# Performance work log

Measured on AMD Instinct MI355X. Metric: run time of the kernel, lower is better.

Reference implementation:

```python
import jax, jax.numpy as jnp
import numpy as np

C = 64
CR = C // 16  # reduction=16 -> query/key channels
B, H, W = 2, 80, 80


def setup_inputs() -> dict:
    key = jax.random.key(0)
    ks = jax.random.split(key, 13)
    s = 0.05
    return {
        "a": jax.random.normal(ks[0], (B, C, H, W), jnp.float32),
        "b": jax.random.normal(ks[1], (B, C, H, W), jnp.float32),
        "c": jax.random.normal(ks[2], (B, C, H, W), jnp.float32),
        # attentionAB (queries from a, keys from b)
        "wq_ab": jax.random.normal(ks[3], (CR, C), jnp.float32) * s,
        "bq_ab": jax.random.normal(ks[4], (CR,), jnp.float32) * s,
        "wk_ab": jax.random.normal(ks[5], (CR, C), jnp.float32) * s,
        "bk_ab": jax.random.normal(ks[6], (CR,), jnp.float32) * s,
        # attentionBC (queries from c, keys from b)
        "wq_bc": jax.random.normal(ks[7], (CR, C), jnp.float32) * s,
        "bq_bc": jax.random.normal(ks[8], (CR,), jnp.float32) * s,
        "wk_bc": jax.random.normal(ks[9], (CR, C), jnp.float32) * s,
        "bk_bc": jax.random.normal(ks[10], (CR,), jnp.float32) * s,
        # outer value conv on b
        "wv": jax.random.normal(ks[11], (C, C), jnp.float32) * s,
        "bv": jax.random.normal(ks[12], (C,), jnp.float32) * s,
    }


def _proj(x_flat, w, bias):
    # conv1x1 on flattened [B, C, N] -> [B, D, N]
    return jnp.einsum("dc,bcn->bdn", w, x_flat) + bias[None, :, None]


def _attention(x1_flat, x2_flat, wq, bq, wk, bk):
    q = _proj(x1_flat, wq, bq)  # [B, CR, N1]
    k = _proj(x2_flat, wk, bk)  # [B, CR, N2]
    scores = jnp.einsum("bdn,bdm->bnm", q, k)  # [B, N1, N2]
    return jax.nn.softmax(scores, axis=-1)


def reference(a, b, c, wq_ab, bq_ab, wk_ab, bk_ab, wq_bc, bq_bc, wk_bc, bk_bc, wv, bv):
    bsz, ch, h, w = b.shape
    n = h * w
    af = a.reshape(bsz, ch, n)
    bf = b.reshape(bsz, ch, n)
    cf = c.reshape(bsz, ch, n)

    attn_ba = _attention(af, bf, wq_ab, bq_ab, wk_ab, bk_ab)  # [B, Na, Nb]
    attn_bc = _attention(cf, bf, wq_bc, bq_bc, wk_bc, bk_bc)  # [B, Nc, Nb]

    values_b = _proj(bf, wv, bv)  # [B, C, Nb]

    # bmm(values_b, attn^T): contract over key positions m (of b)
    enh_ba = jnp.einsum("bcm,bnm->bcn", values_b, attn_ba)
    enh_bc = jnp.einsum("bcm,bnm->bcn", values_b, attn_bc)
    enhanced = (enh_ba + enh_bc) * 0.5
    return enhanced.reshape(bsz, ch, h, w)
```

## Files before the change

### kernel.cpp

```cpp
#include <hip/hip_runtime.h>
#include <hip/hip_bf16.h>

#define NPIX 6400
#define LOG2E 1.44269504088896340736f
#define KH 5
#define KEYS 1280
#define NCH 20
#define QF 2
#define VSTRIDE 136

typedef _Float16 half_t;
typedef _Float16 half4 __attribute__((ext_vector_type(4)));
typedef __fp16 fp16x2 __attribute__((ext_vector_type(2)));
typedef float float4x __attribute__((ext_vector_type(4)));
typedef unsigned long long u64;

__device__ __forceinline__ float fast_exp2(float x) {
    float r;
    asm volatile("v_exp_f32 %0, %1" : "=v"(r) : "v"(x));
    return r;
}

__global__ __launch_bounds__(256) void proj_kernel(
    const float* __restrict__ a, const float* __restrict__ b, const float* __restrict__ c,
    const float* __restrict__ wq_ab, const float* __restrict__ bq_ab,
    const float* __restrict__ wk_ab, const float* __restrict__ bk_ab,
    const float* __restrict__ wq_bc, const float* __restrict__ bq_bc,
    const float* __restrict__ wk_bc, const float* __restrict__ bk_bc,
    const float* __restrict__ wv, const float* __restrict__ bvb,
    half_t* __restrict__ qp, half_t* __restrict__ kp, half_t* __restrict__ vp,
    float* __restrict__ num)
{
    int bid = blockIdx.x;
    if (bid < 400) {
        int tid = bid * 256 + threadIdx.x;
        int n4 = tid % 1600;
        int cc = (tid / 1600) & 31;
        int bz = tid / (1600 * 32);
        const float* B = b + bz * 64 * NPIX + n4 * 4;
        float b0 = bvb[cc], b1 = bvb[cc + 32];
        float4x acc0 = {b0, b0, b0, b0}, acc1 = {b1, b1, b1, b1};
        for (int ch = 0; ch < 64; ++ch) {
            float4x bv = *(const float4x*)(B + ch * NPIX);
            acc0 += wv[cc * 64 + ch] * bv;
            acc1 += wv[(cc + 32) * 64 + ch] * bv;
        }
        half4 h0 = {(half_t)acc0[0], (half_t)acc0[1], (half_t)acc0[2], (half_t)acc0[3]};
        half4 h1 = {(half_t)acc1[0], (half_t)acc1[1], (half_t)acc1[2], (half_t)acc1[3]};
        *(half4*)(vp + (bz * 64 + cc) * NPIX + n4 * 4) = h0;
        *(half4*)(vp + (bz * 64 + cc + 32) * NPIX + n4 * 4) = h1;
    } else if (bid < 600) {
        int tid = (bid - 400) * 256 + threadIdx.x;
        int d = tid & 3;
        int n = (tid >> 2) % NPIX;
        int bz = (tid >> 2) / NPIX;
        const float* A = a + bz * 64 * NPIX + n;
        const float* B = b + bz * 64 * NPIX + n;
        const float* C = c + bz * 64 * NPIX + n;
        float qab = 0.f, kab = 0.f, qbc = 0.f, kbc = 0.f;
#pragma unroll 4
        for (int ch = 0; ch < 64; ++ch) {
            float av = A[ch * NPIX], bv = B[ch * NPIX], cv = C[ch * NPIX];
            qab += wq_ab[d * 64 + ch] * av;
            kab += wk_ab[d * 64 + ch] * bv;
            qbc += wq_bc[d * 64 + ch] * cv;
            kbc += wk_bc[d * 64 + ch] * bv;
        }
        qp[((bz * 2 + 0) * NPIX + n) * 4 + d] = (half_t)((qab + bq_ab[d]) * LOG2E);
        qp[((bz * 2 + 1) * NPIX + n) * 4 + d] = (half_t)((qbc + bq_bc[d]) * LOG2E);
        kp[((bz * 2 + 0) * NPIX + n) * 4 + d] = (half_t)(kab + bk_ab[d]);
        kp[((bz * 2 + 1) * NPIX + n) * 4 + d] = (half_t)(kbc + bk_bc[d]);
    } else {
        int tid = (bid - 600) * 256 + threadIdx.x;
        float4x z = {0.f, 0.f, 0.f, 0.f};
        float4x* p = (float4x*)num;
        for (int i = tid; i < 416000; i += 25600) p[i] = z;
    }
}

__global__ __launch_bounds__(256) void attn_kernel(
    const half_t* __restrict__ qp, const half_t* __restrict__ kp,
    const half_t* __restrict__ vp, float* __restrict__ num, float* __restrict__ lsum)
{
    int bid = blockIdx.x;
    int swz = (bid & 7) * 125 + (bid >> 3);
    int qc = swz % 50;
    int br = (swz / 50) & 1;
    int bz = (swz / 100) & 1;
    int kh = swz / 200;

    int tid = threadIdx.x;
    int lane = tid & 63, w = tid >> 6;
    int g = lane >> 4, qi = lane & 15;
    int qbase = qc * 128 + w * 32;

    const half_t* Q = qp + ((bz * 2 + br) * NPIX + qbase) * 4;
    const half_t* K = kp + ((bz * 2 + br) * NPIX + kh * KEYS) * 4;
    const half_t* V = vp + bz * 64 * NPIX + kh * KEYS;

    half4 hz = {(half_t)0, (half_t)0, (half_t)0, (half_t)0};
    half4 qf[QF];
#pragma unroll
    for (int i = 0; i < QF; ++i)
        qf[i] = (lane < 16) ? *(const half4*)(Q + (i * 16 + lane) * 4) : hz;

    float4x accs[QF][4] = {{{0,0,0,0},{0,0,0,0},{0,0,0,0},{0,0,0,0}},
                           {{0,0,0,0},{0,0,0,0},{0,0,0,0},{0,0,0,0}}};
    float lrun[QF] = {0.f, 0.f};

    __shared__ char lds[2][64 * VSTRIDE];

    u64 vpre[4];
#pragma unroll
    for (int p = 0; p < 4; ++p) {
        int idx = p * 256 + tid; int row = idx >> 4, w4 = idx & 15;
        vpre[p] = *(const u64*)(V + row * NPIX + w4 * 4);
    }
    half4 kc[4];
#pragma unroll
    for (int t = 0; t < 4; ++t)
        kc[t] = (lane < 16) ? *(const half4*)(K + (t * 16 + lane) * 4) : hz;
#pragma unroll
    for (int p = 0; p < 4; ++p) {
        int idx = p * 256 + tid; int row = idx >> 4, w4 = idx & 15;
        *(u64*)(lds[0] + row * VSTRIDE + w4 * 8) = vpre[p];
    }
    __syncthreads();

    int cur = 0;
    for (int chn = 0; chn < NCH; ++chn) {
        bool more = (chn + 1 < NCH);
        u64 vn[4];
        half4 kn[4];
        if (more) {
            int m0n = (chn + 1) * 64;
#pragma unroll
            for (int p = 0; p < 4; ++p) {
                int idx = p * 256 + tid; int row = idx >> 4, w4 = idx & 15;
                vn[p] = *(const u64*)(V + row * NPIX + m0n + w4 * 4);
            }
#pragma unroll
            for (int t = 0; t < 4; ++t)
                kn[t] = (lane < 16) ? *(const half4*)(K + (m0n + t * 16 + lane) * 4) : hz;
        }
        const char* lb = lds[cur];
        half4 vfa[4], vfb[4];
#pragma unroll
        for (int cb = 0; cb < 4; ++cb)
            vfa[cb] = *(const half4*)(lb + (cb * 16 + qi) * VSTRIDE + g * 8);
#pragma unroll
        for (int t = 0; t < 4; ++t) {
            half4* vcur = (t & 1) ? vfb : vfa;
            half4* vnxt = (t & 1) ? vfa : vfb;
            if (t < 3) {
#pragma unroll
                for (int cb = 0; cb < 4; ++cb)
                    vnxt[cb] = *(const half4*)(lb + (cb * 16 + qi) * VSTRIDE + (t + 1) * 32 + g * 8);
            }
#pragma unroll
            for (int i = 0; i < QF; ++i) {
                float4x zero = {0.f, 0.f, 0.f, 0.f};
                float4x sc = __builtin_amdgcn_mfma_f32_16x16x16f16(kc[t], qf[i], zero, 0, 0, 0);
                float p0 = fast_exp2(sc[0]), p1 = fast_exp2(sc[1]);
                float p2 = fast_exp2(sc[2]), p3 = fast_exp2(sc[3]);
                lrun[i] += (p0 + p1) + (p2 + p3);
                union { fp16x2 h2[2]; half4 h4; } pk;
                pk.h2[0] = __builtin_amdgcn_cvt_pkrtz(p0, p1);
                pk.h2[1] = __builtin_amdgcn_cvt_pkrtz(p2, p3);
                half4 pf = pk.h4;
#pragma unroll
                for (int cb = 0; cb < 4; ++cb)
                    accs[i][cb] = __builtin_amdgcn_mfma_f32_16x16x16f16(vcur[cb], pf, accs[i][cb], 0, 0, 0);
            }
        }
        if (more) {
#pragma unroll
            for (int p = 0; p < 4; ++p) {
                int idx = p * 256 + tid; int row = idx >> 4, w4 = idx & 15;
                *(u64*)(lds[cur ^ 1] + row * VSTRIDE + w4 * 8) = vn[p];
            }
#pragma unroll
            for (int t = 0; t < 4; ++t) kc[t] = kn[t];
        }
        __syncthreads();
        cur ^= 1;
    }

    float* numb = num + (bz * 2 + br) * 64 * NPIX;
#pragma unroll
    for (int i = 0; i < QF; ++i) {
        float l = lrun[i];
        l += __shfl_xor(l, 16, 64);
        l += __shfl_xor(l, 32, 64);
        int q = qbase + i * 16 + qi;
        if (g == 0) atomicAdd(&lsum[(bz * 2 + br) * NPIX + q], l);
#pragma unroll
        for (int cb = 0; cb < 4; ++cb)
#pragma unroll
            for (int r = 0; r < 4; ++r)
                atomicAdd(&numb[(cb * 16 + 4 * g + r) * NPIX + q], accs[i][cb][r]);
    }
}

__global__ __launch_bounds__(256) void norm_kernel(
    const float* __restrict__ num, const float* __restrict__ lsum, float* __restrict__ out)
{
    int tid = blockIdx.x * 256 + threadIdx.x;
    int n4 = tid % 1600;
    int c  = (tid / 1600) & 63;
    int bz = tid / (1600 * 64);
    float4x lA = *(const float4x*)(lsum + (bz * 2 + 0) * NPIX + n4 * 4);
    float4x lC = *(const float4x*)(lsum + (bz * 2 + 1) * NPIX + n4 * 4);
    float4x vA = *(const float4x*)(num + ((bz * 2 + 0) * 64 + c) * NPIX + n4 * 4);
    float4x vC = *(const float4x*)(num + ((bz * 2 + 1) * 64 + c) * NPIX + n4 * 4);
    float4x r;
#pragma unroll
    for (int j = 0; j < 4; ++j)
        r[j] = 0.5f * (vA[j] * __builtin_amdgcn_rcpf(lA[j]) +
                       vC[j] * __builtin_amdgcn_rcpf(lC[j]));
    *(float4x*)(out + (bz * 64 + c) * NPIX + n4 * 4) = r;
}

extern "C" void kernel_launch(void* const* d_in, const int* in_sizes, int n_in,
                              void* d_out, int out_size, void* d_ws, size_t ws_size,
                              hipStream_t stream) {
    (void)in_sizes; (void)n_in; (void)out_size; (void)ws_size;
    const float* a     = (const float*)d_in[0];
    const float* b     = (const float*)d_in[1];
    const float* c     = (const float*)d_in[2];
    const float* wq_ab = (const float*)d_in[3];
    const float* bq_ab = (const float*)d_in[4];
    const float* wk_ab = (const float*)d_in[5];
    const float* bk_ab = (const float*)d_in[6];
    const float* wq_bc = (const float*)d_in[7];
    const float* bq_bc = (const float*)d_in[8];
    const float* wk_bc = (const float*)d_in[9];
    const float* bk_bc = (const float*)d_in[10];
    const float* wv    = (const float*)d_in[11];
    const float* bv    = (const float*)d_in[12];
    float* out = (float*)d_out;

    half_t* qp = (half_t*)d_ws;
    half_t* kp = qp + 2 * 2 * NPIX * 4;
    half_t* vp = kp + 2 * 2 * NPIX * 4;
    float* num  = (float*)(vp + 2 * 64 * NPIX);
    float* lsum = num + 2 * 2 * 64 * NPIX;

    proj_kernel<<<700, 256, 0, stream>>>(a, b, c, wq_ab, bq_ab, wk_ab, bk_ab,
                                         wq_bc, bq_bc, wk_bc, bk_bc, wv, bv,
                                         qp, kp, vp, num);
    attn_kernel<<<1000, 256, 0, stream>>>(qp, kp, vp, num, lsum);
    norm_kernel<<<800, 256, 0, stream>>>(num, lsum, out);
}
```

Before: 193.7 us.

## Use MFMA for projections and drop LDS staging in attention kernel

The projection kernel now computes the Q/K/V 1x1 convolutions with fp16 MFMA instructions, one wave per 16 pixels, instead of scalar FMA loops. The attention kernel loads V and K fragments straight from global memory into registers with a one-step prefetch, removing the LDS double buffer and the __syncthreads. Keys are split into 10 chunks instead of 5, doubling the grid to raise parallelism at the cost of more atomic adds into num. Rounding inputs and weights to fp16 in the projections lowers precision.

Result: slower. 259.1 us (+33.7%).

```diff
diff --git a/kernel.cpp b/kernel.cpp
--- a/kernel.cpp
+++ b/kernel.cpp
@@ -3,22 +3,27 @@
 
 #define NPIX 6400
 #define LOG2E 1.44269504088896340736f
-#define KH 5
-#define KEYS 1280
-#define NCH 20
+#define KH 10
+#define KEYS 640
+#define NSTEP 40
 #define QF 2
-#define VSTRIDE 136
 
 typedef _Float16 half_t;
 typedef _Float16 half4 __attribute__((ext_vector_type(4)));
 typedef __fp16 fp16x2 __attribute__((ext_vector_type(2)));
 typedef float float4x __attribute__((ext_vector_type(4)));
-typedef unsigned long long u64;
 
 __device__ __forceinline__ float fast_exp2(float x) {
     float r;
     asm volatile("v_exp_f32 %0, %1" : "=v"(r) : "v"(x));
     return r;
+}
+
+__device__ __forceinline__ half4 cvtf4(float4x v) {
+    union { fp16x2 h2[2]; half4 h4; } u;
+    u.h2[0] = __builtin_amdgcn_cvt_pkrtz(v[0], v[1]);
+    u.h2[1] = __builtin_amdgcn_cvt_pkrtz(v[2], v[3]);
+    return u.h4;
 }
 
 __global__ __launch_bounds__(256) void proj_kernel(
@@ -32,49 +37,88 @@
     float* __restrict__ num)
 {
     int bid = blockIdx.x;
-    if (bid < 400) {
-        int tid = bid * 256 + threadIdx.x;
-        int n4 = tid % 1600;
-        int cc = (tid / 1600) & 31;
-        int bz = tid / (1600 * 32);
-        const float* B = b + bz * 64 * NPIX + n4 * 4;
-        float b0 = bvb[cc], b1 = bvb[cc + 32];
-        float4x acc0 = {b0, b0, b0, b0}, acc1 = {b1, b1, b1, b1};
-        for (int ch = 0; ch < 64; ++ch) {
-            float4x bv = *(const float4x*)(B + ch * NPIX);
-            acc0 += wv[cc * 64 + ch] * bv;
-            acc1 += wv[(cc + 32) * 64 + ch] * bv;
-        }
-        half4 h0 = {(half_t)acc0[0], (half_t)acc0[1], (half_t)acc0[2], (half_t)acc0[3]};
-        half4 h1 = {(half_t)acc1[0], (half_t)acc1[1], (half_t)acc1[2], (half_t)acc1[3]};
-        *(half4*)(vp + (bz * 64 + cc) * NPIX + n4 * 4) = h0;
-        *(half4*)(vp + (bz * 64 + cc + 32) * NPIX + n4 * 4) = h1;
-    } else if (bid < 600) {
-        int tid = (bid - 400) * 256 + threadIdx.x;
-        int d = tid & 3;
-        int n = (tid >> 2) % NPIX;
-        int bz = (tid >> 2) / NPIX;
-        const float* A = a + bz * 64 * NPIX + n;
-        const float* B = b + bz * 64 * NPIX + n;
-        const float* C = c + bz * 64 * NPIX + n;
-        float qab = 0.f, kab = 0.f, qbc = 0.f, kbc = 0.f;
-#pragma unroll 4
-        for (int ch = 0; ch < 64; ++ch) {
-            float av = A[ch * NPIX], bv = B[ch * NPIX], cv = C[ch * NPIX];
-            qab += wq_ab[d * 64 + ch] * av;
-            kab += wk_ab[d * 64 + ch] * bv;
-            qbc += wq_bc[d * 64 + ch] * cv;
-            kbc += wk_bc[d * 64 + ch] * bv;
-        }
-        qp[((bz * 2 + 0) * NPIX + n) * 4 + d] = (half_t)((qab + bq_ab[d]) * LOG2E);
-        qp[((bz * 2 + 1) * NPIX + n) * 4 + d] = (half_t)((qbc + bq_bc[d]) * LOG2E);
-        kp[((bz * 2 + 0) * NPIX + n) * 4 + d] = (half_t)(kab + bk_ab[d]);
-        kp[((bz * 2 + 1) * NPIX + n) * 4 + d] = (half_t)(kbc + bk_bc[d]);
-    } else {
-        int tid = (bid - 600) * 256 + threadIdx.x;
+    int tid = threadIdx.x;
+    if (bid >= 200) {
+        int t = (bid - 200) * 256 + tid;
         float4x z = {0.f, 0.f, 0.f, 0.f};
         float4x* p = (float4x*)num;
-        for (int i = tid; i < 416000; i += 25600) p[i] = z;
+        for (int i = t; i < 416000; i += 16384) p[i] = z;
+        return;
+    }
+    int wid = bid * 4 + (tid >> 6);
+    int lane = tid & 63;
+    int m = lane & 15, g = lane >> 4;
+    int bz = wid / 400;
+    int pix0 = (wid % 400) * 16;
+    const float* Ain = a + bz * 64 * NPIX + pix0 + m;
+    const float* Bin = b + bz * 64 * NPIX + pix0 + m;
+    const float* Cin = c + bz * 64 * NPIX + pix0 + m;
+
+    float4x zf = {0.f, 0.f, 0.f, 0.f};
+    float4x acc_qa = zf, acc_k = zf, acc_qc = zf;
+    float4x acc_v0 = zf, acc_v1 = zf, acc_v2 = zf, acc_v3 = zf;
+    half4 hz = {(half_t)0, (half_t)0, (half_t)0, (half_t)0};
+
+#pragma unroll
+    for (int kt = 0; kt < 4; ++kt) {
+        int ch0 = kt * 16 + g * 4;
+        float4x fa, fb, fc;
+#pragma unroll
+        for (int j = 0; j < 4; ++j) {
+            fa[j] = Ain[(ch0 + j) * NPIX];
+            fb[j] = Bin[(ch0 + j) * NPIX];
+            fc[j] = Cin[(ch0 + j) * NPIX];
+        }
+        half4 ba = cvtf4(fa), bb = cvtf4(fb), bc_ = cvtf4(fc);
+        half4 wa = hz, w0 = hz, wc = hz;
+        if (m < 4) {
+            wa = cvtf4(*(const float4x*)(wq_ab + m * 64 + ch0));
+            w0 = cvtf4(*(const float4x*)(wk_ab + m * 64 + ch0));
+            wc = cvtf4(*(const float4x*)(wq_bc + m * 64 + ch0));
+        } else if (m < 8) {
+            w0 = cvtf4(*(const float4x*)(wk_bc + (m - 4) * 64 + ch0));
+        }
+        acc_qa = __builtin_amdgcn_mfma_f32_16x16x16f16(wa, ba, acc_qa, 0, 0, 0);
+        acc_k  = __builtin_amdgcn_mfma_f32_16x16x16f16(w0, bb, acc_k, 0, 0, 0);
+        acc_qc = __builtin_amdgcn_mfma_f32_16x16x16f16(wc, bc_, acc_qc, 0, 0, 0);
+        half4 wv0 = cvtf4(*(const float4x*)(wv + (0 * 16 + m) * 64 + ch0));
+        acc_v0 = __builtin_amdgcn_mfma_f32_16x16x16f16(wv0, bb, acc_v0, 0, 0, 0);
+        half4 wv1 = cvtf4(*(const float4x*)(wv + (1 * 16 + m) * 64 + ch0));
+        acc_v1 = __builtin_amdgcn_mfma_f32_16x16x16f16(wv1, bb, acc_v1, 0, 0, 0);
+        half4 wv2 = cvtf4(*(const float4x*)(wv + (2 * 16 + m) * 64 + ch0));
+        acc_v2 = __builtin_amdgcn_mfma_f32_16x16x16f16(wv2, bb, acc_v2, 0, 0, 0);
+        half4 wv3 = cvtf4(*(const float4x*)(wv + (3 * 16 + m) * 64 + ch0));
+        acc_v3 = __builtin_amdgcn_mfma_f32_16x16x16f16(wv3, bb, acc_v3, 0, 0, 0);
+    }
+
+    int px = pix0 + m;
+    if (g == 0) {
+        half4 q0, q1, k0;
+#pragma unroll
+        for (int r = 0; r < 4; ++r) {
+            q0[r] = (half_t)((acc_qa[r] + bq_ab[r]) * LOG2E);
+            q1[r] = (half_t)((acc_qc[r] + bq_bc[r]) * LOG2E);
+            k0[r] = (half_t)(acc_k[r] + bk_ab[r]);
+        }
+        *(half4*)(qp + ((bz * 2 + 0) * NPIX + px) * 4) = q0;
+        *(half4*)(qp + ((bz * 2 + 1) * NPIX + px) * 4) = q1;
+        *(half4*)(kp + ((bz * 2 + 0) * NPIX + px) * 4) = k0;
+    } else if (g == 1) {
+        half4 k1;
+#pragma unroll
+        for (int r = 0; r < 4; ++r) k1[r] = (half_t)(acc_k[r] + bk_bc[r]);
+        *(half4*)(kp + ((bz * 2 + 1) * NPIX + px) * 4) = k1;
+    }
+#pragma unroll
+    for (int r = 0; r < 4; ++r) {
+        int c0 = 0 * 16 + 4 * g + r;
+        vp[(bz * 64 + c0) * NPIX + px] = (half_t)(acc_v0[r] + bvb[c0]);
+        int c1 = 1 * 16 + 4 * g + r;
+        vp[(bz * 64 + c1) * NPIX + px] = (half_t)(acc_v1[r] + bvb[c1]);
+        int c2 = 2 * 16 + 4 * g + r;
+        vp[(bz * 64 + c2) * NPIX + px] = (half_t)(acc_v2[r] + bvb[c2]);
+        int c3 = 3 * 16 + 4 * g + r;
+        vp[(bz * 64 + c3) * NPIX + px] = (half_t)(acc_v3[r] + bvb[c3]);
     }
 }
 
@@ -83,7 +127,7 @@
     const half_t* __restrict__ vp, float* __restrict__ num, float* __restrict__ lsum)
 {
     int bid = blockIdx.x;
-    int swz = (bid & 7) * 125 + (bid >> 3);
+    int swz = (bid & 7) * 250 + (bid >> 3);
     int qc = swz % 50;
     int br = (swz / 50) & 1;
     int bz = (swz / 100) & 1;
@@ -108,82 +152,40 @@
                            {{0,0,0,0},{0,0,0,0},{0,0,0,0},{0,0,0,0}}};
     float lrun[QF] = {0.f, 0.f};
 
-    __shared__ char lds[2][64 * VSTRIDE];
-
-    u64 vpre[4];
-#pragma unroll
-    for (int p = 0; p < 4; ++p) {
-        int idx = p * 256 + tid; int row = idx >> 4, w4 = idx & 15;
-        vpre[p] = *(const u64*)(V + row * NPIX + w4 * 4);
-    }
-    half4 kc[4];
-#pragma unroll
-    for (int t = 0; t < 4; ++t)
-        kc[t] = (lane < 16) ? *(const half4*)(K + (t * 16 + lane) * 4) : hz;
-#pragma unroll
-    for (int p = 0; p < 4; ++p) {
-        int idx = p * 256 + tid; int row = idx >> 4, w4 = idx & 15;
-        *(u64*)(lds[0] + row * VSTRIDE + w4 * 8) = vpre[p];
-    }
-    __syncthreads();
-
-    int cur = 0;
-    for (int chn = 0; chn < NCH; ++chn) {
-        bool more = (chn + 1 < NCH);
-        u64 vn[4];
-        half4 kn[4];
+    half4 kc = (lane < 16) ? *(const half4*)(K + lane * 4) : hz;
+    half4 vc0 = *(const half4*)(V + (0 * 16 + qi) * NPIX + g * 4);
+    half4 vc1 = *(const half4*)(V + (1 * 16 + qi) * NPIX + g * 4);
+    half4 vc2 = *(const half4*)(V + (2 * 16 + qi) * NPIX + g * 4);
+    half4 vc3 = *(const half4*)(V + (3 * 16 + qi) * NPIX + g * 4);
+
+    for (int ts = 0; ts < NSTEP; ++ts) {
+        bool more = (ts + 1 < NSTEP);
+        half4 kn = hz, vn0, vn1, vn2, vn3;
         if (more) {
-            int m0n = (chn + 1) * 64;
-#pragma unroll
-            for (int p = 0; p < 4; ++p) {
-                int idx = p * 256 + tid; int row = idx >> 4, w4 = idx & 15;
-                vn[p] = *(const u64*)(V + row * NPIX + m0n + w4 * 4);
-            }
-#pragma unroll
-            for (int t = 0; t < 4; ++t)
-                kn[t] = (lane < 16) ? *(const half4*)(K + (m0n + t * 16 + lane) * 4) : hz;
-        }
-        const char* lb = lds[cur];
-        half4 vfa[4], vfb[4];
-#pragma unroll
-        for (int cb = 0; cb < 4; ++cb)
-            vfa[cb] = *(const half4*)(lb + (cb * 16 + qi) * VSTRIDE + g * 8);
-#pragma unroll
-        for (int t = 0; t < 4; ++t) {
-            half4* vcur = (t & 1) ? vfb : vfa;
-            half4* vnxt = (t & 1) ? vfa : vfb;
-            if (t < 3) {
-#pragma unroll
-                for (int cb = 0; cb < 4; ++cb)
-                    vnxt[cb] = *(const half4*)(lb + (cb * 16 + qi) * VSTRIDE + (t + 1) * 32 + g * 8);
-            }
-#pragma unroll
-            for (int i = 0; i < QF; ++i) {
-                float4x zero = {0.f, 0.f, 0.f, 0.f};
-                float4x sc = __builtin_amdgcn_mfma_f32_16x16x16f16(kc[t], qf[i], zero, 0, 0, 0);
-                float p0 = fast_exp2(sc[0]), p1 = fast_exp2(sc[1]);
-                float p2 = fast_exp2(sc[2]), p3 = fast_exp2(sc[3]);
-                lrun[i] += (p0 + p1) + (p2 + p3);
-                union { fp16x2 h2[2]; half4 h4; } pk;
-                pk.h2[0] = __builtin_amdgcn_cvt_pkrtz(p0, p1);
-                pk.h2[1] = __builtin_amdgcn_cvt_pkrtz(p2, p3);
-                half4 pf = pk.h4;
-#pragma unroll
-                for (int cb = 0; cb < 4; ++cb)
-                    accs[i][cb] = __builtin_amdgcn_mfma_f32_16x16x16f16(vcur[cb], pf, accs[i][cb], 0, 0, 0);
-            }
-        }
-        if (more) {
-#pragma unroll
-            for (int p = 0; p < 4; ++p) {
-                int idx = p * 256 + tid; int row = idx >> 4, w4 = idx & 15;
-                *(u64*)(lds[cur ^ 1] + row * VSTRIDE + w4 * 8) = vn[p];
-            }
-#pragma unroll
-            for (int t = 0; t < 4; ++t) kc[t] = kn[t];
-        }
-        __syncthreads();
-        cur ^= 1;
+            int mt = (ts + 1) * 16;
+            kn = (lane < 16) ? *(const half4*)(K + (mt + lane) * 4) : hz;
+            vn0 = *(const half4*)(V + (0 * 16 + qi) * NPIX + mt + g * 4);
+            vn1 = *(const half4*)(V + (1 * 16 + qi) * NPIX + mt + g * 4);
+            vn2 = *(const half4*)(V + (2 * 16 + qi) * NPIX + mt + g * 4);
+            vn3 = *(const half4*)(V + (3 * 16 + qi) * NPIX + mt + g * 4);
+        }
+#pragma unroll
+        for (int i = 0; i < QF; ++i) {
+            float4x zero = {0.f, 0.f, 0.f, 0.f};
+            float4x sc = __builtin_amdgcn_mfma_f32_16x16x16f16(kc, qf[i], zero, 0, 0, 0);
+            float p0 = fast_exp2(sc[0]), p1 = fast_exp2(sc[1]);
+            float p2 = fast_exp2(sc[2]), p3 = fast_exp2(sc[3]);
+            lrun[i] += (p0 + p1) + (p2 + p3);
+            union { fp16x2 h2[2]; half4 h4; } pk;
+            pk.h2[0] = __builtin_amdgcn_cvt_pkrtz(p0, p1);
+            pk.h2[1] = __builtin_amdgcn_cvt_pkrtz(p2, p3);
+            half4 pf = pk.h4;
+            accs[i][0] = __builtin_amdgcn_mfma_f32_16x16x16f16(vc0, pf, accs[i][0], 0, 0, 0);
+            accs[i][1] = __builtin_amdgcn_mfma_f32_16x16x16f16(vc1, pf, accs[i][1], 0, 0, 0);
+            accs[i][2] = __builtin_amdgcn_mfma_f32_16x16x16f16(vc2, pf, accs[i][2], 0, 0, 0);
+            accs[i][3] = __builtin_amdgcn_mfma_f32_16x16x16f16(vc3, pf, accs[i][3], 0, 0, 0);
+        }
+        kc = kn; vc0 = vn0; vc1 = vn1; vc2 = vn2; vc3 = vn3;
     }
 
     float* numb = num + (bz * 2 + br) * 64 * NPIX;
@@ -246,9 +248,9 @@
     float* num  = (float*)(vp + 2 * 64 * NPIX);
     float* lsum = num + 2 * 2 * 64 * NPIX;
 
-    proj_kernel<<<700, 256, 0, stream>>>(a, b, c, wq_ab, bq_ab, wk_ab, bk_ab,
+    proj_kernel<<<264, 256, 0, stream>>>(a, b, c, wq_ab, bq_ab, wk_ab, bk_ab,
                                          wq_bc, bq_bc, wk_bc, bk_bc, wv, bv,
                                          qp, kp, vp, num);
-    attn_kernel<<<1000, 256, 0, stream>>>(qp, kp, vp, num, lsum);
+    attn_kernel<<<2000, 256, 0, stream>>>(qp, kp, vp, num, lsum);
     norm_kernel<<<800, 256, 0, stream>>>(num, lsum, out);
 }
```
